# Kernel tuning notes

Measured on AMD Instinct MI355X. Metric: run time of the kernel, lower is better.

## Reference

```python
import jax, jax.numpy as jnp
import numpy as np

T, B, E, H = 2048, 2, 1024, 16
Dh = E // H


def setup_inputs() -> dict:
    key = jax.random.key(0)
    ks = jax.random.split(key, 5)
    s = 0.02
    query = jax.random.normal(ks[0], (T, B, E), dtype=jnp.float32)
    Wq = jax.random.normal(ks[1], (E, E), dtype=jnp.float32) * s
    Wk = jax.random.normal(ks[2], (E, E), dtype=jnp.float32) * s
    Wv = jax.random.normal(ks[3], (E, E), dtype=jnp.float32) * s
    Wo = jax.random.normal(ks[4], (E, E), dtype=jnp.float32) * s
    bq = jnp.zeros((E,), jnp.float32)
    bk = jnp.zeros((E,), jnp.float32)
    bv = jnp.zeros((E,), jnp.float32)
    bo = jnp.zeros((E,), jnp.float32)
    # additive causal mask: 0 on/below diagonal, -inf above (standard fairseq usage)
    neg = jnp.finfo(jnp.float32).min
    attn_mask = jnp.where(jnp.triu(jnp.ones((T, T), jnp.bool_), k=1), neg, 0.0).astype(jnp.float32)
    return {"query": query, "Wq": Wq, "bq": bq, "Wk": Wk, "bk": bk,
            "Wv": Wv, "bv": bv, "Wo": Wo, "bo": bo, "attn_mask": attn_mask}


def reference(query, Wq, bq, Wk, bk, Wv, bv, Wo, bo, attn_mask):
    t, b, e = query.shape
    scale = Dh ** -0.5
    # self-attention projections (nn.Linear: x @ W.T + b)
    q = (query @ Wq.T + bq) * scale  # [T,B,E]
    k = query @ Wk.T + bk
    v = query @ Wv.T + bv
    # [T, B*H, Dh] -> [B*H, T, Dh]
    q = q.reshape(t, b * H, Dh).transpose(1, 0, 2)
    k = k.reshape(t, b * H, Dh).transpose(1, 0, 2)
    v = v.reshape(t, b * H, Dh).transpose(1, 0, 2)
    # explicit bmm -> softmax -> bmm (materializes [B*H, T, T])
    attn_weights = jnp.einsum('btd,bsd->bts', q, k) + attn_mask[None, :, :]
    attn_probs = jax.nn.softmax(attn_weights, axis=-1)
    attn = jnp.einsum('bts,bsd->btd', attn_probs, v)  # [B*H, T, Dh]
    attn = attn.transpose(1, 0, 2).reshape(t, b, e)  # [T,B,E]
    out = attn @ Wo.T + bo
    return out
```

## Files before the change

kernel.cpp:

```cpp
#include <hip/hip_runtime.h>


typedef __attribute__((ext_vector_type(8))) short   s16x8;
typedef __attribute__((ext_vector_type(4))) float   f32x4;
typedef __attribute__((ext_vector_type(2))) __fp16  f16x2;
typedef __attribute__((ext_vector_type(4))) __fp16  f16x4;

#define MFMA16(a, b, c) __builtin_amdgcn_mfma_f32_16x16x32_bf16((a), (b), (c), 0, 0, 0)
#define MFMApv(a, b, c) __builtin_amdgcn_mfma_f32_16x16x16f16((a), (b), (c), 0, 0, 0)

static __device__ __forceinline__ unsigned short f2bf(float f) {
    unsigned u = __float_as_uint(f);
    unsigned r = u + 0x7fffu + ((u >> 16) & 1u);
    return (unsigned short)(r >> 16);
}

static __device__ __forceinline__ void gl2lds16(const void* g, void* l) {
    __builtin_amdgcn_global_load_lds(
        (const __attribute__((address_space(1))) unsigned int*)g,
        (__attribute__((address_space(3))) unsigned int*)l, 16, 0, 0);
}

__global__ __launch_bounds__(256) void cvt_all(const float* __restrict__ query,
                                               const float* __restrict__ w0,
                                               const float* __restrict__ w1,
                                               const float* __restrict__ w2,
                                               const float* __restrict__ w3,
                                               unsigned short* __restrict__ Xb,
                                               unsigned short* __restrict__ Wcat) {
    const int bx = blockIdx.x;
    if (bx < 4096) {
        const int i = threadIdx.x;
        const float4 f = reinterpret_cast<const float4*>(query + (size_t)bx * 1024)[i];
        ushort4 u;
        u.x = f2bf(f.x); u.y = f2bf(f.y); u.z = f2bf(f.z); u.w = f2bf(f.w);
        const int mrow = (bx & 1) * 2048 + (bx >> 1);
        reinterpret_cast<ushort4*>(Xb + (size_t)mrow * 1024)[i] = u;
    } else {
        const int j   = bx - 4096;
        const int sel = j >> 10;
        const int i   = (j & 1023) * 256 + threadIdx.x;
        const float* src = (sel == 0) ? w0 : (sel == 1) ? w1 : (sel == 2) ? w2 : w3;
        const float4 f = reinterpret_cast<const float4*>(src)[i];
        ushort4 u;
        u.x = f2bf(f.x); u.y = f2bf(f.y); u.z = f2bf(f.z); u.w = f2bf(f.w);
        reinterpret_cast<ushort4*>(Wcat + (size_t)sel * 1048576)[i] = u;
    }
}

__global__ __launch_bounds__(256) void gemm128(const unsigned short* __restrict__ A,
                                               const unsigned short* __restrict__ W,
                                               const float* __restrict__ b0,
                                               const float* __restrict__ b1,
                                               const float* __restrict__ b2,
                                               unsigned short* __restrict__ outQK,
                                               __fp16* __restrict__ outV,
                                               float* __restrict__ outF,
                                               int qkv) {
    __shared__ __align__(16) unsigned short smem[2][2][128 * 32];

    const int tid  = threadIdx.x;
    const int w    = tid >> 6;
    const int lane = tid & 63;
    const int quad = lane >> 4;
    const int c    = lane & 15;
    const int wm   = w >> 1;
    const int wn   = w & 1;

    const int m0 = blockIdx.y * 128;
    const int n0 = blockIdx.x * 128;

    f32x4 acc[4][4];
    #pragma unroll
    for (int mi = 0; mi < 4; ++mi)
        #pragma unroll
        for (int ni = 0; ni < 4; ++ni) acc[mi][ni] = (f32x4){0.f, 0.f, 0.f, 0.f};

    const int srow = tid >> 2;
    const int sci  = (tid & 3) ^ ((tid >> 3) & 3);
    const unsigned short* aG = A + (size_t)(m0 + srow) * 1024 + sci * 8;
    const unsigned short* wG = W + (size_t)(n0 + srow) * 1024 + sci * 8;
    const int soff = srow * 32 + (tid & 3) * 8;

    const int swz = (quad ^ ((c >> 1) & 3)) * 8;

    gl2lds16(aG,             &smem[0][0][soff]);
    gl2lds16(aG + 64 * 1024, &smem[0][0][soff + 64 * 32]);
    gl2lds16(wG,             &smem[0][1][soff]);
    gl2lds16(wG + 64 * 1024, &smem[0][1][soff + 64 * 32]);

    for (int kk = 0; kk < 32; ++kk) {
        const int buf = kk & 1;
        __syncthreads();
        if (kk + 1 < 32) {
            const int k1 = (kk + 1) * 32;
            const int nb = buf ^ 1;
            gl2lds16(aG + k1,             &smem[nb][0][soff]);
            gl2lds16(aG + k1 + 64 * 1024, &smem[nb][0][soff + 64 * 32]);
            gl2lds16(wG + k1,             &smem[nb][1][soff]);
            gl2lds16(wG + k1 + 64 * 1024, &smem[nb][1][soff + 64 * 32]);
        }

        s16x8 af[4], bf[4];
        #pragma unroll
        for (int mi = 0; mi < 4; ++mi)
            af[mi] = *reinterpret_cast<const s16x8*>(&smem[buf][0][(wm * 64 + mi * 16 + c) * 32 + swz]);
        #pragma unroll
        for (int ni = 0; ni < 4; ++ni)
            bf[ni] = *reinterpret_cast<const s16x8*>(&smem[buf][1][(wn * 64 + ni * 16 + c) * 32 + swz]);
        #pragma unroll
        for (int mi = 0; mi < 4; ++mi)
            #pragma unroll
            for (int ni = 0; ni < 4; ++ni)
                acc[mi][ni] = MFMA16(af[mi], bf[ni], acc[mi][ni]);
    }

    if (qkv) {
        const int sel = n0 >> 10;
        if (sel < 2) {
            const float scale = (sel == 0) ? 0.18033688011112042f : 1.0f;
            const float* bias = (sel == 0) ? b0 : b1;
            #pragma unroll
            for (int ni = 0; ni < 4; ++ni) {
                const int n = n0 + wn * 64 + ni * 16 + c;
                const float bval = bias[n & 1023];
                #pragma unroll
                for (int mi = 0; mi < 4; ++mi)
                    #pragma unroll
                    for (int r = 0; r < 4; ++r) {
                        const int m = m0 + wm * 64 + mi * 16 + quad * 4 + r;
                        outQK[(size_t)m * 2048 + n] = f2bf((acc[mi][ni][r] + bval) * scale);
                    }
            }
        } else {
            __syncthreads();
            unsigned short* tile = &smem[0][0][0];
            #pragma unroll
            for (int ni = 0; ni < 4; ++ni) {
                const int n = wn * 64 + ni * 16 + c;
                const float bval = b2[(n0 - 2048) + n];
                #pragma unroll
                for (int mi = 0; mi < 4; ++mi) {
                    const int m = wm * 64 + mi * 16 + quad * 4;
                    const f16x2 lo = __builtin_amdgcn_cvt_pkrtz(acc[mi][ni][0] + bval,
                                                                acc[mi][ni][1] + bval);
                    const f16x2 hi = __builtin_amdgcn_cvt_pkrtz(acc[mi][ni][2] + bval,
                                                                acc[mi][ni][3] + bval);
                    uint2 st;
                    st.x = __builtin_bit_cast(unsigned int, lo);
                    st.y = __builtin_bit_cast(unsigned int, hi);
                    const int phys = n * 128 + (((m >> 3) ^ (n & 15)) << 3) + (m & 7);
                    *reinterpret_cast<uint2*>(&tile[phys]) = st;
                }
            }
            __syncthreads();
            const int n = tid >> 1;
            const int vcol = (n0 - 2048) + n;
            const int bb = m0 >> 11, tbase = m0 & 2047;
            __fp16* vdst = outV + ((size_t)((bb * 16 + (vcol >> 6)) * 64 + (vcol & 63))) * 2048 + tbase;
            #pragma unroll
            for (int j = 0; j < 8; ++j) {
                const int lc = (tid & 1) * 8 + j;
                const int phys = n * 128 + ((lc ^ (n & 15)) << 3);
                *reinterpret_cast<uint4*>(vdst + lc * 8) =
                    *reinterpret_cast<const uint4*>(&tile[phys]);
            }
        }
    } else {
        #pragma unroll
        for (int ni = 0; ni < 4; ++ni) {
            const int n = n0 + wn * 64 + ni * 16 + c;
            const float bval = b0[n];
            #pragma unroll
            for (int mi = 0; mi < 4; ++mi) {
                const int m = m0 + wm * 64 + mi * 16 + quad * 4;
                const int bb = m >> 11, t = m & 2047;
                #pragma unroll
                for (int r = 0; r < 4; ++r)
                    outF[(size_t)(2 * (t + r) + bb) * 1024 + n] = acc[mi][ni][r] + bval;
            }
        }
    }
}

__global__ __launch_bounds__(256, 2) void attn_kernel(const unsigned short* __restrict__ QKb,
                                                      const __fp16* __restrict__ Vt,
                                                      unsigned short* __restrict__ Ob) {
    __shared__ unsigned short Kl[2][2][64][32];
    __shared__ __fp16 Vl[2][64][64];

    const int tid  = threadIdx.x;
    const int w    = tid >> 6;
    const int lane = tid & 63;
    const int quad = lane >> 4;
    const int c    = lane & 15;

    const int bh = blockIdx.x, bB = bh >> 4, h = bh & 15;
    const int p  = blockIdx.y;
    const int aT[2]   = { 31 - p, p };
    const int trgT[2] = { aT[0] * 64 + w * 16, aT[1] * 64 + w * 16 };
    const int nIt = 32 - p;

    s16x8 aq[2][2];
    #pragma unroll
    for (int t = 0; t < 2; ++t) {
        const unsigned short* qp = QKb + (size_t)(bB * 2048 + trgT[t] + c) * 2048 + h * 64 + quad * 8;
        aq[t][0] = *reinterpret_cast<const s16x8*>(qp);
        aq[t][1] = *reinterpret_cast<const s16x8*>(qp + 32);
    }

    const int lr4 = lane >> 2, sl4 = lane & 3;
    const unsigned short* kSrc = QKb + (size_t)(bB * 2048 + w * 16 + lr4) * 2048
                                 + 1024 + h * 64 + (sl4 ^ ((lane >> 3) & 3)) * 8;
    const int vr8 = lane >> 3, sl8 = lane & 7;
    const __fp16* vSrcA = Vt + (size_t)(bh * 64 + w * 16 + vr8) * 2048 + (sl8 ^ vr8) * 8;
    const __fp16* vSrcB = vSrcA + (size_t)8 * 2048;

    f32x4 acc[2][4];
    float l[2] = {0.f, 0.f};
    #pragma unroll
    for (int t = 0; t < 2; ++t)
        #pragma unroll
        for (int dt = 0; dt < 4; ++dt) acc[t][dt] = (f32x4){0.f, 0.f, 0.f, 0.f};

    const int kswz = (quad ^ ((c >> 1) & 3)) * 8;

    {
        gl2lds16(kSrc,      &Kl[0][0][w * 16 + lr4][sl4 * 8]);
        gl2lds16(kSrc + 32, &Kl[0][1][w * 16 + lr4][sl4 * 8]);
        gl2lds16(vSrcA,     &Vl[0][w * 16 + vr8][sl8 * 8]);
        gl2lds16(vSrcB,     &Vl[0][w * 16 + 8 + vr8][sl8 * 8]);
    }

    for (int it = 0; it < nIt; ++it) {
        const int buf = it & 1;
        __syncthreads();
        if (it + 1 < nIt) {
            const size_t s1 = (size_t)(it + 1) * 64;
            const int nb = buf ^ 1;
            gl2lds16(kSrc + s1 * 2048,      &Kl[nb][0][w * 16 + lr4][sl4 * 8]);
            gl2lds16(kSrc + s1 * 2048 + 32, &Kl[nb][1][w * 16 + lr4][sl4 * 8]);
            gl2lds16(vSrcA + s1,            &Vl[nb][w * 16 + vr8][sl8 * 8]);
            gl2lds16(vSrcB + s1,            &Vl[nb][w * 16 + 8 + vr8][sl8 * 8]);
        }

        s16x8 kf[4][2];
        #pragma unroll
        for (int ns = 0; ns < 4; ++ns) {
            kf[ns][0] = *reinterpret_cast<const s16x8*>(&Kl[buf][0][ns * 16 + c][kswz]);
            kf[ns][1] = *reinterpret_cast<const s16x8*>(&Kl[buf][1][ns * 16 + c][kswz]);
        }
        f16x4 vf[4][4];
        #pragma unroll
        for (int dt = 0; dt < 4; ++dt)
            #pragma unroll
            for (int ch = 0; ch < 4; ++ch) {
                const int phys = ((2 * ch + (quad >> 1)) ^ (c & 7)) * 8 + (quad & 1) * 4;
                vf[dt][ch] = *reinterpret_cast<const f16x4*>(&Vl[buf][dt * 16 + c][phys]);
            }

        const int s0 = it * 64;
        #pragma unroll
        for (int t = 0; t < 2; ++t) {
            if (it > aT[t]) continue;
            const bool diag = (it == aT[t]);
            f32x4 sT[4];
            #pragma unroll
            for (int ns = 0; ns < 4; ++ns) {
                f32x4 z = (f32x4){0.f, 0.f, 0.f, 0.f};
                z = MFMA16(kf[ns][0], aq[t][0], z);
                sT[ns] = MFMA16(kf[ns][1], aq[t][1], z);
            }
            f16x4 pf[4];
            float lp = 0.f;
            #pragma unroll
            for (int ns = 0; ns < 4; ++ns) {
                float pv[4];
                #pragma unroll
                for (int r = 0; r < 4; ++r) pv[r] = exp2f(sT[ns][r]);
                if (diag) {
                    const int sb = s0 + ns * 16 + quad * 4;
                    const int qg = trgT[t] + c;
                    #pragma unroll
                    for (int r = 0; r < 4; ++r) if (sb + r > qg) pv[r] = 0.f;
                }
                lp += (pv[0] + pv[1]) + (pv[2] + pv[3]);
                const f16x2 lo = __builtin_amdgcn_cvt_pkrtz(pv[0], pv[1]);
                const f16x2 hi = __builtin_amdgcn_cvt_pkrtz(pv[2], pv[3]);
                pf[ns] = __builtin_shufflevector(lo, hi, 0, 1, 2, 3);
            }
            l[t] += lp;
            #pragma unroll
            for (int dt = 0; dt < 4; ++dt)
                #pragma unroll
                for (int ns = 0; ns < 4; ++ns)
                    acc[t][dt] = MFMApv(vf[dt][ns], pf[ns], acc[t][dt]);
        }
    }

    #pragma unroll
    for (int t = 0; t < 2; ++t) {
        float lv = l[t];
        lv += __shfl_xor(lv, 16);
        lv += __shfl_xor(lv, 32);
        const float inv = 1.0f / lv;
        const size_t base = (size_t)(bB * 2048 + trgT[t] + c) * 1024 + h * 64;
        #pragma unroll
        for (int dt = 0; dt < 4; ++dt) {
            const unsigned u0 = (unsigned)f2bf(acc[t][dt][0] * inv)
                              | ((unsigned)f2bf(acc[t][dt][1] * inv) << 16);
            const unsigned u1 = (unsigned)f2bf(acc[t][dt][2] * inv)
                              | ((unsigned)f2bf(acc[t][dt][3] * inv) << 16);
            uint2 st; st.x = u0; st.y = u1;
            *reinterpret_cast<uint2*>(Ob + base + dt * 16 + quad * 4) = st;
        }
    }
}

extern "C" void kernel_launch(void* const* d_in, const int* in_sizes, int n_in,
                              void* d_out, int out_size, void* d_ws, size_t ws_size,
                              hipStream_t stream) {
    const float* query = (const float*)d_in[0];
    const float* Wq    = (const float*)d_in[1];
    const float* bq    = (const float*)d_in[2];
    const float* Wk    = (const float*)d_in[3];
    const float* bk    = (const float*)d_in[4];
    const float* Wv    = (const float*)d_in[5];
    const float* bv    = (const float*)d_in[6];
    const float* Wo    = (const float*)d_in[7];
    const float* bo    = (const float*)d_in[8];

    float* out = (float*)d_out;

    unsigned short* ws    = (unsigned short*)d_ws;
    unsigned short* Xbf   = ws;
    unsigned short* Wcat  = Xbf  + (size_t)4096 * 1024;
    unsigned short* QKb   = Wcat + (size_t)4 * 1024 * 1024;
    __fp16*         Vtw   = (__fp16*)(QKb + (size_t)4096 * 2048);
    unsigned short* attnb = (unsigned short*)(Vtw + (size_t)32 * 64 * 2048);

    cvt_all<<<8192, 256, 0, stream>>>(query, Wq, Wk, Wv, Wo, Xbf, Wcat);

    gemm128<<<dim3(24, 32), 256, 0, stream>>>(Xbf, Wcat, bq, bk, bv,
                                              QKb, Vtw, nullptr, 1);

    attn_kernel<<<dim3(32, 16), 256, 0, stream>>>(QKb, Vtw, attnb);

    gemm128<<<dim3(8, 32), 256, 0, stream>>>(attnb, Wcat + (size_t)3 * 1024 * 1024,
                                             bo, nullptr, nullptr, nullptr, nullptr, out, 0);
}
```

Baseline: 211.0 us.

## Split GEMMs, drop LDS double buffering, one q-tile per attention block

The shared GEMM is split into a QKV-specific kernel and an output-projection kernel. The QKV GEMM drops LDS double buffering in favour of a single buffer with two barriers per k-step. The output GEMM uses 64x128 tiles, doubling the block count. The attention kernel no longer pairs two query tiles per block to balance the causal work; it launches one block per query tile with launch bounds raised to 4 waves per SIMD. These changes trade latency hiding and load balance for lower LDS and register use, higher occupancy and more blocks. Heavy-first block ordering (31 - blockIdx.y) is relied on to keep the causal workload balanced.

```diff
diff --git a/kernel.cpp b/kernel.cpp
--- a/kernel.cpp
+++ b/kernel.cpp
@@ -48,16 +48,16 @@
     }
 }
 
-__global__ __launch_bounds__(256) void gemm128(const unsigned short* __restrict__ A,
-                                               const unsigned short* __restrict__ W,
-                                               const float* __restrict__ b0,
-                                               const float* __restrict__ b1,
-                                               const float* __restrict__ b2,
-                                               unsigned short* __restrict__ outQK,
-                                               __fp16* __restrict__ outV,
-                                               float* __restrict__ outF,
-                                               int qkv) {
-    __shared__ __align__(16) unsigned short smem[2][2][128 * 32];
+__global__ __launch_bounds__(256) void gemm_qkv(const unsigned short* __restrict__ A,
+                                                const unsigned short* __restrict__ W,
+                                                const float* __restrict__ b0,
+                                                const float* __restrict__ b1,
+                                                const float* __restrict__ b2,
+                                                unsigned short* __restrict__ outQK,
+                                                __fp16* __restrict__ outV) {
+    __shared__ __align__(16) unsigned short smem[16384];
+    unsigned short* Al = smem;
+    unsigned short* Bl = smem + 4096;
 
     const int tid  = threadIdx.x;
     const int w    = tid >> 6;
@@ -84,30 +84,22 @@
 
     const int swz = (quad ^ ((c >> 1) & 3)) * 8;
 
-    gl2lds16(aG,             &smem[0][0][soff]);
-    gl2lds16(aG + 64 * 1024, &smem[0][0][soff + 64 * 32]);
-    gl2lds16(wG,             &smem[0][1][soff]);
-    gl2lds16(wG + 64 * 1024, &smem[0][1][soff + 64 * 32]);
-
     for (int kk = 0; kk < 32; ++kk) {
-        const int buf = kk & 1;
-        __syncthreads();
-        if (kk + 1 < 32) {
-            const int k1 = (kk + 1) * 32;
-            const int nb = buf ^ 1;
-            gl2lds16(aG + k1,             &smem[nb][0][soff]);
-            gl2lds16(aG + k1 + 64 * 1024, &smem[nb][0][soff + 64 * 32]);
-            gl2lds16(wG + k1,             &smem[nb][1][soff]);
-            gl2lds16(wG + k1 + 64 * 1024, &smem[nb][1][soff + 64 * 32]);
-        }
+        const int k0 = kk * 32;
+        __syncthreads();
+        gl2lds16(aG + k0,             &Al[soff]);
+        gl2lds16(aG + k0 + 64 * 1024, &Al[soff + 64 * 32]);
+        gl2lds16(wG + k0,             &Bl[soff]);
+        gl2lds16(wG + k0 + 64 * 1024, &Bl[soff + 64 * 32]);
+        __syncthreads();
 
         s16x8 af[4], bf[4];
         #pragma unroll
         for (int mi = 0; mi < 4; ++mi)
-            af[mi] = *reinterpret_cast<const s16x8*>(&smem[buf][0][(wm * 64 + mi * 16 + c) * 32 + swz]);
+            af[mi] = *reinterpret_cast<const s16x8*>(&Al[(wm * 64 + mi * 16 + c) * 32 + swz]);
         #pragma unroll
         for (int ni = 0; ni < 4; ++ni)
-            bf[ni] = *reinterpret_cast<const s16x8*>(&smem[buf][1][(wn * 64 + ni * 16 + c) * 32 + swz]);
+            bf[ni] = *reinterpret_cast<const s16x8*>(&Bl[(wn * 64 + ni * 16 + c) * 32 + swz]);
         #pragma unroll
         for (int mi = 0; mi < 4; ++mi)
             #pragma unroll
@@ -115,79 +107,63 @@
                 acc[mi][ni] = MFMA16(af[mi], bf[ni], acc[mi][ni]);
     }
 
-    if (qkv) {
-        const int sel = n0 >> 10;
-        if (sel < 2) {
-            const float scale = (sel == 0) ? 0.18033688011112042f : 1.0f;
-            const float* bias = (sel == 0) ? b0 : b1;
-            #pragma unroll
-            for (int ni = 0; ni < 4; ++ni) {
-                const int n = n0 + wn * 64 + ni * 16 + c;
-                const float bval = bias[n & 1023];
-                #pragma unroll
-                for (int mi = 0; mi < 4; ++mi)
-                    #pragma unroll
-                    for (int r = 0; r < 4; ++r) {
-                        const int m = m0 + wm * 64 + mi * 16 + quad * 4 + r;
-                        outQK[(size_t)m * 2048 + n] = f2bf((acc[mi][ni][r] + bval) * scale);
-                    }
-            }
-        } else {
-            __syncthreads();
-            unsigned short* tile = &smem[0][0][0];
-            #pragma unroll
-            for (int ni = 0; ni < 4; ++ni) {
-                const int n = wn * 64 + ni * 16 + c;
-                const float bval = b2[(n0 - 2048) + n];
-                #pragma unroll
-                for (int mi = 0; mi < 4; ++mi) {
-                    const int m = wm * 64 + mi * 16 + quad * 4;
-                    const f16x2 lo = __builtin_amdgcn_cvt_pkrtz(acc[mi][ni][0] + bval,
-                                                                acc[mi][ni][1] + bval);
-                    const f16x2 hi = __builtin_amdgcn_cvt_pkrtz(acc[mi][ni][2] + bval,
-                                                                acc[mi][ni][3] + bval);
-                    uint2 st;
-                    st.x = __builtin_bit_cast(unsigned int, lo);
-                    st.y = __builtin_bit_cast(unsigned int, hi);
-                    const int phys = n * 128 + (((m >> 3) ^ (n & 15)) << 3) + (m & 7);
-                    *reinterpret_cast<uint2*>(&tile[phys]) = st;
-                }
-            }
-            __syncthreads();
-            const int n = tid >> 1;
-            const int vcol = (n0 - 2048) + n;
-            const int bb = m0 >> 11, tbase = m0 & 2047;
-            __fp16* vdst = outV + ((size_t)((bb * 16 + (vcol >> 6)) * 64 + (vcol & 63))) * 2048 + tbase;
-            #pragma unroll
-            for (int j = 0; j < 8; ++j) {
-                const int lc = (tid & 1) * 8 + j;
-                const int phys = n * 128 + ((lc ^ (n & 15)) << 3);
-                *reinterpret_cast<uint4*>(vdst + lc * 8) =
-                    *reinterpret_cast<const uint4*>(&tile[phys]);
-            }
-        }
-    } else {
+    const int sel = n0 >> 10;
+    if (sel < 2) {
+        const float scale = (sel == 0) ? 0.18033688011112042f : 1.0f;
+        const float* bias = (sel == 0) ? b0 : b1;
         #pragma unroll
         for (int ni = 0; ni < 4; ++ni) {
             const int n = n0 + wn * 64 + ni * 16 + c;
-            const float bval = b0[n];
+            const float bval = bias[n & 1023];
+            #pragma unroll
+            for (int mi = 0; mi < 4; ++mi)
+                #pragma unroll
+                for (int r = 0; r < 4; ++r) {
+                    const int m = m0 + wm * 64 + mi * 16 + quad * 4 + r;
+                    outQK[(size_t)m * 2048 + n] = f2bf((acc[mi][ni][r] + bval) * scale);
+                }
+        }
+    } else {
+        __syncthreads();
+        #pragma unroll
+        for (int ni = 0; ni < 4; ++ni) {
+            const int n = wn * 64 + ni * 16 + c;
+            const float bval = b2[(n0 - 2048) + n];
             #pragma unroll
             for (int mi = 0; mi < 4; ++mi) {
-                const int m = m0 + wm * 64 + mi * 16 + quad * 4;
-                const int bb = m >> 11, t = m & 2047;
-                #pragma unroll
-                for (int r = 0; r < 4; ++r)
-                    outF[(size_t)(2 * (t + r) + bb) * 1024 + n] = acc[mi][ni][r] + bval;
+                const int m = wm * 64 + mi * 16 + quad * 4;
+                const f16x2 lo = __builtin_amdgcn_cvt_pkrtz(acc[mi][ni][0] + bval,
+                                                            acc[mi][ni][1] + bval);
+                const f16x2 hi = __builtin_amdgcn_cvt_pkrtz(acc[mi][ni][2] + bval,
+                                                            acc[mi][ni][3] + bval);
+                uint2 st;
+                st.x = __builtin_bit_cast(unsigned int, lo);
+                st.y = __builtin_bit_cast(unsigned int, hi);
+                const int phys = n * 128 + (((m >> 3) ^ (n & 15)) << 3) + (m & 7);
+                *reinterpret_cast<uint2*>(&smem[phys]) = st;
             }
         }
-    }
-}
-
-__global__ __launch_bounds__(256, 2) void attn_kernel(const unsigned short* __restrict__ QKb,
-                                                      const __fp16* __restrict__ Vt,
-                                                      unsigned short* __restrict__ Ob) {
-    __shared__ unsigned short Kl[2][2][64][32];
-    __shared__ __fp16 Vl[2][64][64];
+        __syncthreads();
+        const int n = tid >> 1;
+        const int vcol = (n0 - 2048) + n;
+        const int bb = m0 >> 11, tbase = m0 & 2047;
+        __fp16* vdst = outV + ((size_t)((bb * 16 + (vcol >> 6)) * 64 + (vcol & 63))) * 2048 + tbase;
+        #pragma unroll
+        for (int j = 0; j < 8; ++j) {
+            const int lc = (tid & 1) * 8 + j;
+            const int phys = n * 128 + ((lc ^ (n & 15)) << 3);
+            *reinterpret_cast<uint4*>(vdst + lc * 8) =
+                *reinterpret_cast<const uint4*>(&smem[phys]);
+        }
+    }
+}
+
+__global__ __launch_bounds__(256) void gemm_out(const unsigned short* __restrict__ A,
+                                                const unsigned short* __restrict__ W,
+                                                const float* __restrict__ bias,
+                                                float* __restrict__ outF) {
+    __shared__ __align__(16) unsigned short Al[64 * 32];
+    __shared__ __align__(16) unsigned short Bl[128 * 32];
 
     const int tid  = threadIdx.x;
     const int w    = tid >> 6;
@@ -195,19 +171,70 @@
     const int quad = lane >> 4;
     const int c    = lane & 15;
 
+    const int m0 = blockIdx.y * 64;
+    const int n0 = blockIdx.x * 128;
+
+    f32x4 acc[8];
+    #pragma unroll
+    for (int ni = 0; ni < 8; ++ni) acc[ni] = (f32x4){0.f, 0.f, 0.f, 0.f};
+
+    const int srow = tid >> 2;
+    const int sci  = (tid & 3) ^ ((tid >> 3) & 3);
+    const unsigned short* aG = A + (size_t)(m0 + srow) * 1024 + sci * 8;
+    const unsigned short* wG = W + (size_t)(n0 + srow) * 1024 + sci * 8;
+    const int aoff = srow * 32 + (tid & 3) * 8;
+
+    const int swz = (quad ^ ((c >> 1) & 3)) * 8;
+
+    for (int kk = 0; kk < 32; ++kk) {
+        const int k0 = kk * 32;
+        __syncthreads();
+        gl2lds16(aG + k0,             &Al[aoff]);
+        gl2lds16(wG + k0,             &Bl[aoff]);
+        gl2lds16(wG + k0 + 64 * 1024, &Bl[aoff + 64 * 32]);
+        __syncthreads();
+
+        const s16x8 af = *reinterpret_cast<const s16x8*>(&Al[(w * 16 + c) * 32 + swz]);
+        #pragma unroll
+        for (int ni = 0; ni < 8; ++ni) {
+            const s16x8 bf = *reinterpret_cast<const s16x8*>(&Bl[(ni * 16 + c) * 32 + swz]);
+            acc[ni] = MFMA16(af, bf, acc[ni]);
+        }
+    }
+
+    #pragma unroll
+    for (int ni = 0; ni < 8; ++ni) {
+        const int n = n0 + ni * 16 + c;
+        const float bval = bias[n];
+        const int m = m0 + w * 16 + quad * 4;
+        const int bb = m >> 11, t = m & 2047;
+        #pragma unroll
+        for (int r = 0; r < 4; ++r)
+            outF[(size_t)(2 * (t + r) + bb) * 1024 + n] = acc[ni][r] + bval;
+    }
+}
+
+__global__ __launch_bounds__(256, 4) void attn_kernel(const unsigned short* __restrict__ QKb,
+                                                      const __fp16* __restrict__ Vt,
+                                                      unsigned short* __restrict__ Ob) {
+    __shared__ unsigned short Kl[2][2][64][32];
+    __shared__ __fp16 Vl[2][64][64];
+
+    const int tid  = threadIdx.x;
+    const int w    = tid >> 6;
+    const int lane = tid & 63;
+    const int quad = lane >> 4;
+    const int c    = lane & 15;
+
     const int bh = blockIdx.x, bB = bh >> 4, h = bh & 15;
-    const int p  = blockIdx.y;
-    const int aT[2]   = { 31 - p, p };
-    const int trgT[2] = { aT[0] * 64 + w * 16, aT[1] * 64 + w * 16 };
-    const int nIt = 32 - p;
-
-    s16x8 aq[2][2];
-    #pragma unroll
-    for (int t = 0; t < 2; ++t) {
-        const unsigned short* qp = QKb + (size_t)(bB * 2048 + trgT[t] + c) * 2048 + h * 64 + quad * 8;
-        aq[t][0] = *reinterpret_cast<const s16x8*>(qp);
-        aq[t][1] = *reinterpret_cast<const s16x8*>(qp + 32);
-    }
+    const int a  = 31 - (int)blockIdx.y;
+    const int t0 = a * 64;
+    const int trg = t0 + w * 16;
+    const int nIt = a + 1;
+
+    const unsigned short* qp = QKb + (size_t)(bB * 2048 + trg + c) * 2048 + h * 64 + quad * 8;
+    const s16x8 aq0 = *reinterpret_cast<const s16x8*>(qp);
+    const s16x8 aq1 = *reinterpret_cast<const s16x8*>(qp + 32);
 
     const int lr4 = lane >> 2, sl4 = lane & 3;
     const unsigned short* kSrc = QKb + (size_t)(bB * 2048 + w * 16 + lr4) * 2048
@@ -216,12 +243,10 @@
     const __fp16* vSrcA = Vt + (size_t)(bh * 64 + w * 16 + vr8) * 2048 + (sl8 ^ vr8) * 8;
     const __fp16* vSrcB = vSrcA + (size_t)8 * 2048;
 
-    f32x4 acc[2][4];
-    float l[2] = {0.f, 0.f};
-    #pragma unroll
-    for (int t = 0; t < 2; ++t)
-        #pragma unroll
-        for (int dt = 0; dt < 4; ++dt) acc[t][dt] = (f32x4){0.f, 0.f, 0.f, 0.f};
+    f32x4 acc[4];
+    float l = 0.f;
+    #pragma unroll
+    for (int dt = 0; dt < 4; ++dt) acc[dt] = (f32x4){0.f, 0.f, 0.f, 0.f};
 
     const int kswz = (quad ^ ((c >> 1) & 3)) * 8;
 
@@ -260,60 +285,53 @@
             }
 
         const int s0 = it * 64;
-        #pragma unroll
-        for (int t = 0; t < 2; ++t) {
-            if (it > aT[t]) continue;
-            const bool diag = (it == aT[t]);
-            f32x4 sT[4];
-            #pragma unroll
-            for (int ns = 0; ns < 4; ++ns) {
-                f32x4 z = (f32x4){0.f, 0.f, 0.f, 0.f};
-                z = MFMA16(kf[ns][0], aq[t][0], z);
-                sT[ns] = MFMA16(kf[ns][1], aq[t][1], z);
+        const bool diag = (it == a);
+        f32x4 sT[4];
+        #pragma unroll
+        for (int ns = 0; ns < 4; ++ns) {
+            f32x4 z = (f32x4){0.f, 0.f, 0.f, 0.f};
+            z = MFMA16(kf[ns][0], aq0, z);
+            sT[ns] = MFMA16(kf[ns][1], aq1, z);
+        }
+        f16x4 pf[4];
+        float lp = 0.f;
+        #pragma unroll
+        for (int ns = 0; ns < 4; ++ns) {
+            float pv[4];
+            #pragma unroll
+            for (int r = 0; r < 4; ++r) pv[r] = exp2f(sT[ns][r]);
+            if (diag) {
+                const int sb = s0 + ns * 16 + quad * 4;
+                const int qg = trg + c;
+                #pragma unroll
+                for (int r = 0; r < 4; ++r) if (sb + r > qg) pv[r] = 0.f;
             }
-            f16x4 pf[4];
-            float lp = 0.f;
-            #pragma unroll
-            for (int ns = 0; ns < 4; ++ns) {
-                float pv[4];
-                #pragma unroll
-                for (int r = 0; r < 4; ++r) pv[r] = exp2f(sT[ns][r]);
-                if (diag) {
-                    const int sb = s0 + ns * 16 + quad * 4;
-                    const int qg = trgT[t] + c;
-                    #pragma unroll
-                    for (int r = 0; r < 4; ++r) if (sb + r > qg) pv[r] = 0.f;
-                }
-                lp += (pv[0] + pv[1]) + (pv[2] + pv[3]);
-                const f16x2 lo = __builtin_amdgcn_cvt_pkrtz(pv[0], pv[1]);
-                const f16x2 hi = __builtin_amdgcn_cvt_pkrtz(pv[2], pv[3]);
-                pf[ns] = __builtin_shufflevector(lo, hi, 0, 1, 2, 3);
-            }
-            l[t] += lp;
-            #pragma unroll
-            for (int dt = 0; dt < 4; ++dt)
-                #pragma unroll
-                for (int ns = 0; ns < 4; ++ns)
-                    acc[t][dt] = MFMApv(vf[dt][ns], pf[ns], acc[t][dt]);
-        }
-    }
-
-    #pragma unroll
-    for (int t = 0; t < 2; ++t) {
-        float lv = l[t];
-        lv += __shfl_xor(lv, 16);
-        lv += __shfl_xor(lv, 32);
-        const float inv = 1.0f / lv;
-        const size_t base = (size_t)(bB * 2048 + trgT[t] + c) * 1024 + h * 64;
-        #pragma unroll
-        for (int dt = 0; dt < 4; ++dt) {
-            const unsigned u0 = (unsigned)f2bf(acc[t][dt][0] * inv)
-                              | ((unsigned)f2bf(acc[t][dt][1] * inv) << 16);
-            const unsigned u1 = (unsigned)f2bf(acc[t][dt][2] * inv)
-                              | ((unsigned)f2bf(acc[t][dt][3] * inv) << 16);
-            uint2 st; st.x = u0; st.y = u1;
-            *reinterpret_cast<uint2*>(Ob + base + dt * 16 + quad * 4) = st;
-        }
+            lp += (pv[0] + pv[1]) + (pv[2] + pv[3]);
+            const f16x2 lo = __builtin_amdgcn_cvt_pkrtz(pv[0], pv[1]);
+            const f16x2 hi = __builtin_amdgcn_cvt_pkrtz(pv[2], pv[3]);
+            pf[ns] = __builtin_shufflevector(lo, hi, 0, 1, 2, 3);
+        }
+        l += lp;
+        #pragma unroll
+        for (int dt = 0; dt < 4; ++dt)
+            #pragma unroll
+            for (int ns = 0; ns < 4; ++ns)
+                acc[dt] = MFMApv(vf[dt][ns], pf[ns], acc[dt]);
+    }
+
+    float lv = l;
+    lv += __shfl_xor(lv, 16);
+    lv += __shfl_xor(lv, 32);
+    const float inv = 1.0f / lv;
+    const size_t base = (size_t)(bB * 2048 + trg + c) * 1024 + h * 64;
+    #pragma unroll
+    for (int dt = 0; dt < 4; ++dt) {
+        const unsigned u0 = (unsigned)f2bf(acc[dt][0] * inv)
+                          | ((unsigned)f2bf(acc[dt][1] * inv) << 16);
+        const unsigned u1 = (unsigned)f2bf(acc[dt][2] * inv)
+                          | ((unsigned)f2bf(acc[dt][3] * inv) << 16);
+        uint2 st; st.x = u0; st.y = u1;
+        *reinterpret_cast<uint2*>(Ob + base + dt * 16 + quad * 4) = st;
     }
 }
 
@@ -341,11 +359,10 @@
 
     cvt_all<<<8192, 256, 0, stream>>>(query, Wq, Wk, Wv, Wo, Xbf, Wcat);
 
-    gemm128<<<dim3(24, 32), 256, 0, stream>>>(Xbf, Wcat, bq, bk, bv,
-                                              QKb, Vtw, nullptr, 1);
-
-    attn_kernel<<<dim3(32, 16), 256, 0, stream>>>(QKb, Vtw, attnb);
-
-    gemm128<<<dim3(8, 32), 256, 0, stream>>>(attnb, Wcat + (size_t)3 * 1024 * 1024,
-                                             bo, nullptr, nullptr, nullptr, nullptr, out, 0);
-}
+    gemm_qkv<<<dim3(24, 32), 256, 0, stream>>>(Xbf, Wcat, bq, bk, bv, QKb, Vtw);
+
+    attn_kernel<<<dim3(32, 32), 256, 0, stream>>>(QKb, Vtw, attnb);
+
+    gemm_out<<<dim3(8, 64), 256, 0, stream>>>(attnb, Wcat + (size_t)3 * 1024 * 1024,
+                                              bo, out);
+}
```

Measured after the change: 209.5 us. Within noise of the previous version (-0.8%).
